# Performance work log

Measured on AMD Instinct MI355X. Metric: run time of the kernel, lower is better.

## Reference

```python
import jax, jax.numpy as jnp
import numpy as np

WINDOW_SIZE = 11
C1 = (0.01 * 255) ** 2
C2 = (0.03 * 255) ** 2


def _make_window():
    # NOTE: faithful to the torch module: Gaussian with 2*sigma^2 = 4, UNNORMALIZED.
    x = np.arange(WINDOW_SIZE)
    g = np.exp(-((x - WINDOW_SIZE // 2) ** 2) / float(2 * 2)).astype(np.float32)
    w2d = np.outer(g, g)  # [11, 11]
    return jnp.asarray(w2d)[None, None, :, :]  # OIHW = [1, 1, 11, 11]


def _conv(x, w):
    pad = WINDOW_SIZE // 2
    return jax.lax.conv_general_dilated(
        x, w, window_strides=(1, 1), padding=[(pad, pad), (pad, pad)],
        dimension_numbers=('NCHW', 'OIHW', 'NCHW'))


def setup_inputs() -> dict:
    key = jax.random.key(0)
    k1, k2 = jax.random.split(key)
    shape = (32, 1, 512, 512)
    img1 = jax.random.uniform(k1, shape, dtype=jnp.float32)
    img2 = jax.random.uniform(k2, shape, dtype=jnp.float32)
    return {"img1": img1, "img2": img2}


def reference(img1, img2):
    w = _make_window()
    mu1 = _conv(img1, w)
    mu2 = _conv(img2, w)
    mu1_sq = mu1 * mu1
    mu2_sq = mu2 * mu2
    mu1_mu2 = mu1 * mu2
    sigma1_sq = _conv(img1 * img1, w) - mu1_sq
    sigma2_sq = _conv(img2 * img2, w) - mu2_sq
    sigma12 = _conv(img1 * img2, w) - mu1_mu2
    ssim_map = ((2 * mu1_mu2 + C1) * (2 * sigma12 + C2)) / (
        (mu1_sq + mu2_sq + C1) * (sigma1_sq + sigma2_sq + C2))
    return jnp.mean((1.0 - ssim_map) / 2.0)
```

## Files before the change

### kernel.cpp

```cpp
#include <hip/hip_runtime.h>
#include <hip/hip_fp16.h>


#define IMGW 512
#define IMGH 512
#define NIMG 32
#define TW 32
#define TH 64
#define IN_H 74
#define IN_W 44
#define HSTR 36
#define NPIX (IN_H * IN_W)
#define NCHUNK (IN_H * 11)
#define NBX 16
#define NBY 8
#define NBLOCKS (NBX * NBY * NIMG)
#define NT 512
#define LOWCH 512
#define LOWROWS 46

typedef __attribute__((address_space(1))) const uint32_t ga_u32;
typedef __attribute__((address_space(3))) uint32_t ls_u32;

__device__ __forceinline__ void load16_lds(const float* g, float* l) {
  __builtin_amdgcn_global_load_lds((ga_u32*)g, (ls_u32*)l, 16, 0, 0);
}
__device__ __forceinline__ __half2 h2_of(uint32_t w) {
  return __builtin_bit_cast(__half2, w);
}
__device__ __forceinline__ uint32_t u_of(__half2 h) {
  return __builtin_bit_cast(uint32_t, h);
}
__device__ __forceinline__ void lds_barrier() {
  asm volatile("s_waitcnt lgkmcnt(0)" ::: "memory");
  __builtin_amdgcn_s_barrier();
  __builtin_amdgcn_sched_barrier(0);
}

__global__ __launch_bounds__(NT, 8) void ssim_main(
    const float* __restrict__ img1, const float* __restrict__ img2,
    float* __restrict__ partial) {
  __shared__ uint32_t uRaw[NPIX * 2];
  __shared__ uint32_t sPK[NPIX];
  __shared__ float sWave[8];
  float* sA = (float*)uRaw;
  float* sB = (float*)(uRaw + NPIX);
  uint32_t* hAB = uRaw;
  uint32_t* hPM = uRaw + NPIX;

  constexpr float g[11] = {0.0019304541f, 0.018315639f, 0.10539922f,
                           0.36787944f,   0.7788008f,   1.0f,
                           0.7788008f,    0.36787944f,  0.10539922f,
                           0.018315639f,  0.0019304541f};

  __half2 gh[11], gh8[11];
#pragma unroll
  for (int k = 0; k < 11; ++k) {
    gh[k] = __float2half2_rn(g[k]);
    gh8[k] = __float2half2_rn(g[k] * 0.125f);
  }
  const __half2 c1m1 = __floats2half2_rn(1.0f, -1.0f);
  const __half2 kQS = __float2half2_rn(0.0625f);
  const __half2 kQD = __float2half2_rn(0.03125f);
  const __half2 C1s = __float2half2_rn(6.5025f / 64.0f);
  const __half2 C2s = __float2half2_rn(58.5225f / 64.0f);
  const __half2 htwo = __float2half2_rn(2.0f);

  const int tid = threadIdx.x;
  const int bid = blockIdx.x;
  const int wgid = (bid & 7) * (NBLOCKS / 8) + (bid >> 3);
  const int img = wgid >> 7;
  const int by = (wgid >> 4) & 7;
  const int bx = wgid & 15;
  const int x0 = bx * TW - 5;
  const int y0 = by * TH - 5;
  const float* __restrict__ p1 = img1 + (size_t)img * (IMGW * IMGH);
  const float* __restrict__ p2 = img2 + (size_t)img * (IMGW * IMGH);
  const bool borderBlk =
      (bx == 0) || (bx == NBX - 1) || (by == 0) || (by == NBY - 1);

#pragma unroll
  for (int i = 0; i < 2; ++i) {
    int ch = tid + NT * i;
    if (ch >= NCHUNK) ch = tid;
    int r = ch / 11;
    int cg = ch - r * 11;
    int gy = y0 + r;
    int gx = x0 + 4 * cg;
    int gyc = min(max(gy, 0), IMGH - 1);
    int gxc = min(max(gx, 0), IMGW - 4);
    int src = gyc * IMGW + gxc;
    load16_lds(p1 + src, &sA[ch * 4]);
    load16_lds(p2 + src, &sB[ch * 4]);
  }
  asm volatile("s_waitcnt vmcnt(2)" ::: "memory");
  __builtin_amdgcn_s_barrier();
  __builtin_amdgcn_sched_barrier(0);

  auto prepass = [&](int cbeg, int cend) {
    if (!borderBlk) {
      for (int ch = cbeg + tid; ch < cend; ch += NT) {
        float4 a = *(const float4*)&sA[ch * 4];
        float4 b = *(const float4*)&sB[ch * 4];
        uint4 w;
        w.x = u_of(__floats2half2_rn(a.x, b.x));
        w.y = u_of(__floats2half2_rn(a.y, b.y));
        w.z = u_of(__floats2half2_rn(a.z, b.z));
        w.w = u_of(__floats2half2_rn(a.w, b.w));
        *(uint4*)&sPK[ch * 4] = w;
      }
    } else {
      for (int ch = cbeg + tid; ch < cend; ch += NT) {
        int r = ch / 11;
        int cg = ch - r * 11;
        int gy = y0 + r;
        int gx = x0 + 4 * cg;
        float4 a = *(const float4*)&sA[ch * 4];
        float4 b = *(const float4*)&sB[ch * 4];
        bool rowok = (gy >= 0) && (gy < IMGH);
        uint4 w;
        float av[4] = {a.x, a.y, a.z, a.w};
        float bv[4] = {b.x, b.y, b.z, b.w};
        uint32_t* wp = (uint32_t*)&w;
#pragma unroll
        for (int j = 0; j < 4; ++j) {
          bool ok = rowok && (gx + j >= 0) && (gx + j < IMGW);
          wp[j] = u_of(__floats2half2_rn(ok ? av[j] : 0.f, ok ? bv[j] : 0.f));
        }
        *(uint4*)&sPK[ch * 4] = w;
      }
    }
  };

  auto stage2 = [&](int rowbase, int nrows) {
    for (int idx = tid; idx < nrows * 4; idx += NT) {
      int r = rowbase + (idx >> 2);
      int c0 = (idx & 3) << 3;
      int base = r * IN_W + c0;
      __half2 ab[18], pm2[18];
      {
        uint4 w0 = *(const uint4*)&sPK[base];
        uint4 w1 = *(const uint4*)&sPK[base + 4];
        uint4 w2 = *(const uint4*)&sPK[base + 8];
        uint4 w3 = *(const uint4*)&sPK[base + 12];
        uint2 w4 = *(const uint2*)&sPK[base + 16];
        uint32_t ws[18] = {w0.x, w0.y, w0.z, w0.w, w1.x, w1.y, w1.z, w1.w,
                           w2.x, w2.y, w2.z, w2.w, w3.x, w3.y, w3.z, w3.w,
                           w4.x, w4.y};
#pragma unroll
        for (int k = 0; k < 18; ++k) {
          __half2 w = h2_of(ws[k]);
          ab[k] = w;
          __half2 t = __hfma2(__lowhigh2highlow(w), c1m1, w);
          pm2[k] = __hmul2(t, t);
        }
      }
      uint32_t oab[8], opm[8];
#pragma unroll
      for (int o = 0; o < 8; ++o) {
        __half2 cab = __float2half2_rn(0.0f);
        __half2 cpm = __float2half2_rn(0.0f);
#pragma unroll
        for (int k = 0; k < 11; ++k) {
          cab = __hfma2(gh[k], ab[o + k], cab);
          cpm = __hfma2(gh[k], pm2[o + k], cpm);
        }
        oab[o] = u_of(cab);
        opm[o] = u_of(cpm);
      }
      int hb = r * HSTR + c0;
      *(uint4*)&hAB[hb] = make_uint4(oab[0], oab[1], oab[2], oab[3]);
      *(uint4*)&hAB[hb + 4] = make_uint4(oab[4], oab[5], oab[6], oab[7]);
      *(uint4*)&hPM[hb] = make_uint4(opm[0], opm[1], opm[2], opm[3]);
      *(uint4*)&hPM[hb + 4] = make_uint4(opm[4], opm[5], opm[6], opm[7]);
    }
  };

  prepass(0, LOWCH);
  lds_barrier();
  stage2(0, LOWROWS);
  asm volatile("s_waitcnt vmcnt(0) lgkmcnt(0)" ::: "memory");
  __builtin_amdgcn_s_barrier();
  __builtin_amdgcn_sched_barrier(0);
  prepass(LOWCH, NCHUNK);
  lds_barrier();
  stage2(LOWROWS, IN_H - LOWROWS);
  lds_barrier();

  const int cp = tid & 15;
  const int rg = tid >> 4;
  const int r0 = rg << 1;
  __half2 aAB0[2], aAB1[2], aPM0[2], aPM1[2];
#pragma unroll
  for (int o = 0; o < 2; ++o) {
    aAB0[o] = __float2half2_rn(0.f);
    aAB1[o] = __float2half2_rn(0.f);
    aPM0[o] = __float2half2_rn(0.f);
    aPM1[o] = __float2half2_rn(0.f);
  }
#pragma unroll
  for (int k = 0; k < 12; ++k) {
    int row = r0 + k;
    uint2 ab = *(const uint2*)&hAB[row * HSTR + 2 * cp];
    uint2 pm = *(const uint2*)&hPM[row * HSTR + 2 * cp];
#pragma unroll
    for (int o = 0; o < 2; ++o) {
      if (k - o >= 0 && k - o <= 10) {
        aAB0[o] = __hfma2(gh8[k - o], h2_of(ab.x), aAB0[o]);
        aAB1[o] = __hfma2(gh8[k - o], h2_of(ab.y), aAB1[o]);
        aPM0[o] = __hfma2(gh8[k - o], h2_of(pm.x), aPM0[o]);
        aPM1[o] = __hfma2(gh8[k - o], h2_of(pm.y), aPM1[o]);
      }
    }
  }

  float ssum = 0.f;
#pragma unroll
  for (int o = 0; o < 2; ++o) {
    uint32_t uab0 = u_of(aAB0[o]), uab1 = u_of(aAB1[o]);
    uint32_t upm0 = u_of(aPM0[o]), upm1 = u_of(aPM1[o]);
    __half2 M1 = h2_of(__builtin_amdgcn_perm(uab1, uab0, 0x05040100));
    __half2 M2 = h2_of(__builtin_amdgcn_perm(uab1, uab0, 0x07060302));
    __half2 QP = h2_of(__builtin_amdgcn_perm(upm1, upm0, 0x05040100));
    __half2 QM = h2_of(__builtin_amdgcn_perm(upm1, upm0, 0x07060302));
    __half2 m12 = __hmul2(M1, M2);
    __half2 s1q = __hmul2(M1, M1);
    __half2 s2q = __hmul2(M2, M2);
    __half2 sumsq = __hmul2(__hadd2(QP, QM), kQS);
    __half2 eab = __hmul2(__hsub2(QP, QM), kQD);
    __half2 sg12 = __hsub2(eab, m12);
    __half2 sgsum = __hsub2(__hsub2(sumsq, s1q), s2q);
    __half2 numA = __hfma2(m12, htwo, C1s);
    __half2 numB = __hfma2(sg12, htwo, C2s);
    __half2 num = __hmul2(numA, numB);
    __half2 denA = __hadd2(__hadd2(s1q, s2q), C1s);
    __half2 denB = __hadd2(sgsum, C2s);
    __half2 den = __hmul2(denA, denB);
    float nlo = __low2float(num), nhi = __high2float(num);
    float dlo = __low2float(den), dhi = __high2float(den);
    float ra = nlo * __builtin_amdgcn_rcpf(dlo);
    float rb = nhi * __builtin_amdgcn_rcpf(dhi);
    if (!__builtin_isfinite(ra)) ra = 0.f;
    if (!__builtin_isfinite(rb)) rb = 0.f;
    ssum += ra + rb;
  }

#pragma unroll
  for (int off = 32; off > 0; off >>= 1) ssum += __shfl_down(ssum, off, 64);
  if ((tid & 63) == 0) sWave[tid >> 6] = ssum;
  __syncthreads();
  if (tid == 0) {
    float t = 0.f;
#pragma unroll
    for (int w = 0; w < 8; ++w) t += sWave[w];
    partial[wgid] = t;
  }
}

__global__ __launch_bounds__(256) void ssim_reduce(
    const float* __restrict__ partial, float* __restrict__ out) {
  const int tid = threadIdx.x;
  float s = 0.f;
  for (int i = tid; i < NBLOCKS; i += 256) s += partial[i];
#pragma unroll
  for (int off = 32; off > 0; off >>= 1) s += __shfl_down(s, off, 64);
  __shared__ float sw[4];
  if ((tid & 63) == 0) sw[tid >> 6] = s;
  __syncthreads();
  if (tid == 0) {
    float tot = sw[0] + sw[1] + sw[2] + sw[3];
    float val = 0.5f * (1.0f - tot * (1.0f / (32.0f * 512.0f * 512.0f)));
    if (!__builtin_isfinite(val)) val = 0.0f;
    out[0] = val;
  }
}

extern "C" void kernel_launch(void* const* d_in, const int* in_sizes, int n_in,
                              void* d_out, int out_size, void* d_ws,
                              size_t ws_size, hipStream_t stream) {
  const float* img1 = (const float*)d_in[0];
  const float* img2 = (const float*)d_in[1];
  float* partial = (float*)d_ws;
  float* out = (float*)d_out;

  hipLaunchKernelGGL(ssim_main, dim3(NBLOCKS), dim3(NT), 0, stream, img1,
                     img2, partial);
  hipLaunchKernelGGL(ssim_reduce, dim3(1), dim3(256), 0, stream, partial, out);
}
```

Measured before the change: 40.10 us.

## Warp-specialize stages so horizontal and vertical passes overlap across wave groups

```diff
diff --git a/kernel.cpp b/kernel.cpp
--- a/kernel.cpp
+++ b/kernel.cpp
@@ -11,13 +11,12 @@
 #define IN_W 44
 #define HSTR 36
 #define NPIX (IN_H * IN_W)
+#define NPIXA 3328
 #define NCHUNK (IN_H * 11)
 #define NBX 16
 #define NBY 8
 #define NBLOCKS (NBX * NBY * NIMG)
 #define NT 512
-#define LOWCH 512
-#define LOWROWS 46
 
 typedef __attribute__((address_space(1))) const uint32_t ga_u32;
 typedef __attribute__((address_space(3))) uint32_t ls_u32;
@@ -40,13 +39,13 @@
 __global__ __launch_bounds__(NT, 8) void ssim_main(
     const float* __restrict__ img1, const float* __restrict__ img2,
     float* __restrict__ partial) {
-  __shared__ uint32_t uRaw[NPIX * 2];
+  __shared__ uint32_t uRaw[NPIXA * 2];
   __shared__ uint32_t sPK[NPIX];
   __shared__ float sWave[8];
   float* sA = (float*)uRaw;
-  float* sB = (float*)(uRaw + NPIX);
+  float* sB = (float*)(uRaw + NPIXA);
   uint32_t* hAB = uRaw;
-  uint32_t* hPM = uRaw + NPIX;
+  uint32_t* hPM = uRaw + NPIXA;
 
   constexpr float g[11] = {0.0019304541f, 0.018315639f, 0.10539922f,
                            0.36787944f,   0.7788008f,   1.0f,
@@ -67,6 +66,7 @@
   const __half2 htwo = __float2half2_rn(2.0f);
 
   const int tid = threadIdx.x;
+  const int wid = tid >> 6;
   const int bid = blockIdx.x;
   const int wgid = (bid & 7) * (NBLOCKS / 8) + (bid >> 3);
   const int img = wgid >> 7;
@@ -79,61 +79,61 @@
   const bool borderBlk =
       (bx == 0) || (bx == NBX - 1) || (by == 0) || (by == NBY - 1);
 
-#pragma unroll
-  for (int i = 0; i < 2; ++i) {
-    int ch = tid + NT * i;
-    if (ch >= NCHUNK) ch = tid;
+  auto src_of = [&](int ch) {
     int r = ch / 11;
     int cg = ch - r * 11;
     int gy = y0 + r;
     int gx = x0 + 4 * cg;
     int gyc = min(max(gy, 0), IMGH - 1);
     int gxc = min(max(gx, 0), IMGW - 4);
-    int src = gyc * IMGW + gxc;
+    return gyc * IMGW + gxc;
+  };
+
+  {
+    int src = src_of(tid);
+    load16_lds(p1 + src, &sA[tid * 4]);
+    load16_lds(p2 + src, &sB[tid * 4]);
+  }
+  if (wid < 5) {
+    int ch = 512 + tid;
+    int src = src_of(min(ch, NCHUNK - 1));
     load16_lds(p1 + src, &sA[ch * 4]);
     load16_lds(p2 + src, &sB[ch * 4]);
-  }
-  asm volatile("s_waitcnt vmcnt(2)" ::: "memory");
-  __builtin_amdgcn_s_barrier();
+    asm volatile("s_waitcnt vmcnt(2)" ::: "memory");
+  } else {
+    asm volatile("s_waitcnt vmcnt(0)" ::: "memory");
+  }
   __builtin_amdgcn_sched_barrier(0);
 
-  auto prepass = [&](int cbeg, int cend) {
+  auto prepass_chunk = [&](int ch) {
+    float4 a = *(const float4*)&sA[ch * 4];
+    float4 b = *(const float4*)&sB[ch * 4];
+    uint4 w;
     if (!borderBlk) {
-      for (int ch = cbeg + tid; ch < cend; ch += NT) {
-        float4 a = *(const float4*)&sA[ch * 4];
-        float4 b = *(const float4*)&sB[ch * 4];
-        uint4 w;
-        w.x = u_of(__floats2half2_rn(a.x, b.x));
-        w.y = u_of(__floats2half2_rn(a.y, b.y));
-        w.z = u_of(__floats2half2_rn(a.z, b.z));
-        w.w = u_of(__floats2half2_rn(a.w, b.w));
-        *(uint4*)&sPK[ch * 4] = w;
-      }
+      w.x = u_of(__floats2half2_rn(a.x, b.x));
+      w.y = u_of(__floats2half2_rn(a.y, b.y));
+      w.z = u_of(__floats2half2_rn(a.z, b.z));
+      w.w = u_of(__floats2half2_rn(a.w, b.w));
     } else {
-      for (int ch = cbeg + tid; ch < cend; ch += NT) {
-        int r = ch / 11;
-        int cg = ch - r * 11;
-        int gy = y0 + r;
-        int gx = x0 + 4 * cg;
-        float4 a = *(const float4*)&sA[ch * 4];
-        float4 b = *(const float4*)&sB[ch * 4];
-        bool rowok = (gy >= 0) && (gy < IMGH);
-        uint4 w;
-        float av[4] = {a.x, a.y, a.z, a.w};
-        float bv[4] = {b.x, b.y, b.z, b.w};
-        uint32_t* wp = (uint32_t*)&w;
-#pragma unroll
-        for (int j = 0; j < 4; ++j) {
-          bool ok = rowok && (gx + j >= 0) && (gx + j < IMGW);
-          wp[j] = u_of(__floats2half2_rn(ok ? av[j] : 0.f, ok ? bv[j] : 0.f));
-        }
-        *(uint4*)&sPK[ch * 4] = w;
+      int r = ch / 11;
+      int cg = ch - r * 11;
+      int gy = y0 + r;
+      int gx = x0 + 4 * cg;
+      bool rowok = (gy >= 0) && (gy < IMGH);
+      float av[4] = {a.x, a.y, a.z, a.w};
+      float bv[4] = {b.x, b.y, b.z, b.w};
+      uint32_t* wp = (uint32_t*)&w;
+#pragma unroll
+      for (int j = 0; j < 4; ++j) {
+        bool ok = rowok && (gx + j >= 0) && (gx + j < IMGW);
+        wp[j] = u_of(__floats2half2_rn(ok ? av[j] : 0.f, ok ? bv[j] : 0.f));
       }
     }
-  };
-
-  auto stage2 = [&](int rowbase, int nrows) {
-    for (int idx = tid; idx < nrows * 4; idx += NT) {
+    *(uint4*)&sPK[ch * 4] = w;
+  };
+
+  auto stage2 = [&](int rowbase, int nrows, int tbase, int tcnt) {
+    for (int idx = tid - tbase; idx < nrows * 4; idx += tcnt) {
       int r = rowbase + (idx >> 2);
       int c0 = (idx & 3) << 3;
       int base = r * IN_W + c0;
@@ -176,74 +176,78 @@
     }
   };
 
-  prepass(0, LOWCH);
+  float ssum = 0.f;
+  auto stage3 = [&](int r0base, int ngroups, int tbase, int tcnt) {
+    for (int t = tid - tbase; t < ngroups * 16; t += tcnt) {
+      int cp = t & 15;
+      int r0 = r0base + ((t >> 4) << 1);
+      __half2 aAB0[2], aAB1[2], aPM0[2], aPM1[2];
+#pragma unroll
+      for (int o = 0; o < 2; ++o) {
+        aAB0[o] = __float2half2_rn(0.f);
+        aAB1[o] = __float2half2_rn(0.f);
+        aPM0[o] = __float2half2_rn(0.f);
+        aPM1[o] = __float2half2_rn(0.f);
+      }
+#pragma unroll
+      for (int k = 0; k < 12; ++k) {
+        int row = r0 + k;
+        uint2 ab = *(const uint2*)&hAB[row * HSTR + 2 * cp];
+        uint2 pm = *(const uint2*)&hPM[row * HSTR + 2 * cp];
+#pragma unroll
+        for (int o = 0; o < 2; ++o) {
+          if (k - o >= 0 && k - o <= 10) {
+            aAB0[o] = __hfma2(gh8[k - o], h2_of(ab.x), aAB0[o]);
+            aAB1[o] = __hfma2(gh8[k - o], h2_of(ab.y), aAB1[o]);
+            aPM0[o] = __hfma2(gh8[k - o], h2_of(pm.x), aPM0[o]);
+            aPM1[o] = __hfma2(gh8[k - o], h2_of(pm.y), aPM1[o]);
+          }
+        }
+      }
+#pragma unroll
+      for (int o = 0; o < 2; ++o) {
+        uint32_t uab0 = u_of(aAB0[o]), uab1 = u_of(aAB1[o]);
+        uint32_t upm0 = u_of(aPM0[o]), upm1 = u_of(aPM1[o]);
+        __half2 M1 = h2_of(__builtin_amdgcn_perm(uab1, uab0, 0x05040100));
+        __half2 M2 = h2_of(__builtin_amdgcn_perm(uab1, uab0, 0x07060302));
+        __half2 QP = h2_of(__builtin_amdgcn_perm(upm1, upm0, 0x05040100));
+        __half2 QM = h2_of(__builtin_amdgcn_perm(upm1, upm0, 0x07060302));
+        __half2 m12 = __hmul2(M1, M2);
+        __half2 s1q = __hmul2(M1, M1);
+        __half2 s2q = __hmul2(M2, M2);
+        __half2 sumsq = __hmul2(__hadd2(QP, QM), kQS);
+        __half2 eab = __hmul2(__hsub2(QP, QM), kQD);
+        __half2 sg12 = __hsub2(eab, m12);
+        __half2 sgsum = __hsub2(__hsub2(sumsq, s1q), s2q);
+        __half2 num = __hmul2(__hfma2(m12, htwo, C1s), __hfma2(sg12, htwo, C2s));
+        __half2 den = __hmul2(__hadd2(__hadd2(s1q, s2q), C1s),
+                              __hadd2(sgsum, C2s));
+        float ra = __low2float(num) * __builtin_amdgcn_rcpf(__low2float(den));
+        float rb = __high2float(num) * __builtin_amdgcn_rcpf(__high2float(den));
+        if (!__builtin_isfinite(ra)) ra = 0.f;
+        if (!__builtin_isfinite(rb)) rb = 0.f;
+        ssum += ra + rb;
+      }
+    }
+  };
+
+  prepass_chunk(tid);
   lds_barrier();
-  stage2(0, LOWROWS);
-  asm volatile("s_waitcnt vmcnt(0) lgkmcnt(0)" ::: "memory");
-  __builtin_amdgcn_s_barrier();
-  __builtin_amdgcn_sched_barrier(0);
-  prepass(LOWCH, NCHUNK);
+  if (wid < 5) {
+    asm volatile("s_waitcnt vmcnt(0)" ::: "memory");
+    __builtin_amdgcn_sched_barrier(0);
+    if (tid < 302) prepass_chunk(512 + tid);
+  } else {
+    stage2(0, 46, 320, 192);
+  }
   lds_barrier();
-  stage2(LOWROWS, IN_H - LOWROWS);
+  if (wid < 5) {
+    stage3(0, 18, 0, 320);
+  } else {
+    stage2(46, 28, 320, 192);
+  }
   lds_barrier();
-
-  const int cp = tid & 15;
-  const int rg = tid >> 4;
-  const int r0 = rg << 1;
-  __half2 aAB0[2], aAB1[2], aPM0[2], aPM1[2];
-#pragma unroll
-  for (int o = 0; o < 2; ++o) {
-    aAB0[o] = __float2half2_rn(0.f);
-    aAB1[o] = __float2half2_rn(0.f);
-    aPM0[o] = __float2half2_rn(0.f);
-    aPM1[o] = __float2half2_rn(0.f);
-  }
-#pragma unroll
-  for (int k = 0; k < 12; ++k) {
-    int row = r0 + k;
-    uint2 ab = *(const uint2*)&hAB[row * HSTR + 2 * cp];
-    uint2 pm = *(const uint2*)&hPM[row * HSTR + 2 * cp];
-#pragma unroll
-    for (int o = 0; o < 2; ++o) {
-      if (k - o >= 0 && k - o <= 10) {
-        aAB0[o] = __hfma2(gh8[k - o], h2_of(ab.x), aAB0[o]);
-        aAB1[o] = __hfma2(gh8[k - o], h2_of(ab.y), aAB1[o]);
-        aPM0[o] = __hfma2(gh8[k - o], h2_of(pm.x), aPM0[o]);
-        aPM1[o] = __hfma2(gh8[k - o], h2_of(pm.y), aPM1[o]);
-      }
-    }
-  }
-
-  float ssum = 0.f;
-#pragma unroll
-  for (int o = 0; o < 2; ++o) {
-    uint32_t uab0 = u_of(aAB0[o]), uab1 = u_of(aAB1[o]);
-    uint32_t upm0 = u_of(aPM0[o]), upm1 = u_of(aPM1[o]);
-    __half2 M1 = h2_of(__builtin_amdgcn_perm(uab1, uab0, 0x05040100));
-    __half2 M2 = h2_of(__builtin_amdgcn_perm(uab1, uab0, 0x07060302));
-    __half2 QP = h2_of(__builtin_amdgcn_perm(upm1, upm0, 0x05040100));
-    __half2 QM = h2_of(__builtin_amdgcn_perm(upm1, upm0, 0x07060302));
-    __half2 m12 = __hmul2(M1, M2);
-    __half2 s1q = __hmul2(M1, M1);
-    __half2 s2q = __hmul2(M2, M2);
-    __half2 sumsq = __hmul2(__hadd2(QP, QM), kQS);
-    __half2 eab = __hmul2(__hsub2(QP, QM), kQD);
-    __half2 sg12 = __hsub2(eab, m12);
-    __half2 sgsum = __hsub2(__hsub2(sumsq, s1q), s2q);
-    __half2 numA = __hfma2(m12, htwo, C1s);
-    __half2 numB = __hfma2(sg12, htwo, C2s);
-    __half2 num = __hmul2(numA, numB);
-    __half2 denA = __hadd2(__hadd2(s1q, s2q), C1s);
-    __half2 denB = __hadd2(sgsum, C2s);
-    __half2 den = __hmul2(denA, denB);
-    float nlo = __low2float(num), nhi = __high2float(num);
-    float dlo = __low2float(den), dhi = __high2float(den);
-    float ra = nlo * __builtin_amdgcn_rcpf(dlo);
-    float rb = nhi * __builtin_amdgcn_rcpf(dhi);
-    if (!__builtin_isfinite(ra)) ra = 0.f;
-    if (!__builtin_isfinite(rb)) rb = 0.f;
-    ssum += ra + rb;
-  }
+  stage3(36, 14, 0, NT);
 
 #pragma unroll
   for (int off = 32; off > 0; off >>= 1) ssum += __shfl_down(ssum, off, 64);
```

New measurement: 38.90 us. 3.0% less time.
